# Kernel tuning notes

Measured on AMD Instinct MI355X. Metric: run time of the kernel, lower is better.

The kernel has to match this reference:

```python
import jax, jax.numpy as jnp
import numpy as np

VOCAB = 100000
DIM = 128
BATCH = 16384
NEG = 20
REG = 1e-06


def setup_inputs() -> dict:
    key = jax.random.key(0)
    k1, k2, k3, k4, k5, k6 = jax.random.split(key, 6)
    initrange = 0.5 / DIM
    u_emb = jax.random.uniform(k1, (VOCAB, DIM), jnp.float32, -initrange, initrange)
    # torch init is zeros for v; use small noise so the math is non-degenerate
    v_emb = 0.01 * jax.random.normal(k2, (VOCAB, DIM), jnp.float32)
    # pretrained embeddings given to init_emd (constant numpy array in torch)
    pretrained = jax.random.uniform(k3, (VOCAB, DIM), jnp.float32, -initrange, initrange)
    u_pos = jax.random.randint(k4, (BATCH,), 0, VOCAB)
    v_pos = jax.random.randint(k5, (BATCH,), 0, VOCAB)
    v_neg = jax.random.randint(k6, (BATCH, NEG), 0, VOCAB)
    return {"u_emb": u_emb, "v_emb": v_emb, "pretrained": pretrained,
            "u_pos": u_pos, "v_pos": v_pos, "v_neg": v_neg, "batch_size": BATCH}


def reference(u_emb, v_emb, pretrained, u_pos, v_pos, v_neg, batch_size):
    embed_u = u_emb[u_pos]                      # [B, D]
    embed_v = v_emb[v_pos]                      # [B, D]
    score = jnp.sum(embed_u * embed_v, axis=1)  # [B]
    log_target = jax.nn.log_sigmoid(score)      # [B]

    neg_embed_v = v_emb[v_neg]                              # [B, N, D]
    neg_score = jnp.einsum('bnd,bd->bn', neg_embed_v, embed_u)  # [B, N]
    sum_log_sampled = jnp.sum(jax.nn.log_sigmoid(-neg_score), axis=1)  # [B]

    loss = log_target + sum_log_sampled          # [B]

    # Original python loop: for each j in u_pos, loss += reg * sum|U[j]-P[j]|
    # (scalar broadcast-added to the whole [B] vector each iteration).
    reg_total = REG * jnp.sum(jnp.abs(embed_u - pretrained[u_pos]))  # scalar
    loss = loss + reg_total                      # broadcast, same as the loop

    return -jnp.sum(loss) / batch_size
```

## Files before the change

### kernel.cpp

```cpp
#include <hip/hip_runtime.h>
#include <math.h>

#define NEGS 20
#define DIMS 128
#define REGC 1e-6f
#define LPR  16
#define RPW  4

__device__ __forceinline__ float log_sigmoid(float x) {
    float t = __expf(-fabsf(x));
    float l = -__logf(1.f + t);
    return x >= 0.f ? l : x + l;
}

__device__ __forceinline__ float dot4(float4 a, float4 b) {
    return a.x*b.x + a.y*b.y + a.z*b.z + a.w*b.w;
}

__global__ __launch_bounds__(256) void sg_loss_kernel(
    const float* __restrict__ u_emb,
    const float* __restrict__ v_emb,
    const float* __restrict__ pretrained,
    const int* __restrict__ u_pos,
    const int* __restrict__ v_pos,
    const int* __restrict__ v_neg,
    float* __restrict__ out,
    int batch)
{
    const int lane = threadIdx.x & 63;
    const int l    = lane & (LPR - 1);
    const int g    = lane >> 4;
    const int wib  = threadIdx.x >> 6;
    const int wpb  = blockDim.x >> 6;
    const int gwave  = blockIdx.x * wpb + wib;
    const int nwaves = gridDim.x * wpb;

    float s1 = 0.f;
    float s2 = 0.f;

    for (int base = gwave * RPW; base < batch; base += nwaves * RPW) {
        const int  b     = base + g;
        const bool valid = (b < batch);
        const int  ib    = valid ? b : 0;

        const int iu = u_pos[ib];
        const int iv = v_pos[ib];

        int negidx[NEGS];
        #pragma unroll
        for (int n = 0; n < NEGS; ++n) negidx[n] = v_neg[ib * NEGS + n];

        const float4* up = (const float4*)(u_emb      + (size_t)iu * DIMS);
        const float4* vp = (const float4*)(v_emb      + (size_t)iv * DIMS);
        const float4* pp = (const float4*)(pretrained + (size_t)iu * DIMS);
        const float4 u0 = up[l], u1 = up[l + 16];
        const float4 v0 = vp[l], v1 = vp[l + 16];
        const float4 p0 = pp[l], p1 = pp[l + 16];

        float part[NEGS + 1];
        part[0] = dot4(u0, v0) + dot4(u1, v1);
        #pragma unroll
        for (int n = 0; n < NEGS; ++n) {
            const float4* np = (const float4*)(v_emb + (size_t)negidx[n] * DIMS);
            const float4 a = np[l], c = np[l + 16];
            part[n + 1] = dot4(u0, a) + dot4(u1, c);
        }
        float rp = fabsf(u0.x - p0.x) + fabsf(u0.y - p0.y)
                 + fabsf(u0.z - p0.z) + fabsf(u0.w - p0.w)
                 + fabsf(u1.x - p1.x) + fabsf(u1.y - p1.y)
                 + fabsf(u1.z - p1.z) + fabsf(u1.w - p1.w);

        #pragma unroll
        for (int off = 8; off > 0; off >>= 1) {
            #pragma unroll
            for (int k = 0; k <= NEGS; ++k) part[k] += __shfl_xor(part[k], off, 16);
            rp += __shfl_xor(rp, off, 16);
        }

        float acc = log_sigmoid(part[0]);
        #pragma unroll
        for (int n = 0; n < NEGS; ++n) acc += log_sigmoid(-part[n + 1]);

        if (!valid) { acc = 0.f; rp = 0.f; }
        s1 += acc;
        s2 += rp;
    }

    s1 += __shfl_xor(s1, 16, 64);  s2 += __shfl_xor(s2, 16, 64);
    s1 += __shfl_xor(s1, 32, 64);  s2 += __shfl_xor(s2, 32, 64);

    __shared__ float ls1[8], ls2[8];
    if (lane == 0) { ls1[wib] = s1; ls2[wib] = s2; }
    __syncthreads();
    if (threadIdx.x == 0) {
        float t1 = 0.f, t2 = 0.f;
        for (int w = 0; w < wpb; ++w) { t1 += ls1[w]; t2 += ls2[w]; }
        const float contrib = -(t1 / (float)batch) - REGC * t2;
        atomicAdd(out, contrib);
    }
}

extern "C" void kernel_launch(void* const* d_in, const int* in_sizes, int n_in,
                              void* d_out, int out_size, void* d_ws, size_t ws_size,
                              hipStream_t stream) {
    const float* u_emb      = (const float*)d_in[0];
    const float* v_emb      = (const float*)d_in[1];
    const float* pretrained = (const float*)d_in[2];
    const int*   u_pos      = (const int*)d_in[3];
    const int*   v_pos      = (const int*)d_in[4];
    const int*   v_neg      = (const int*)d_in[5];
    float* out = (float*)d_out;
    const int batch = in_sizes[3];

    hipMemsetAsync(out, 0, sizeof(float), stream);

    dim3 block(256);
    int nwaves = (batch + RPW - 1) / RPW;
    int blocks = (nwaves + 3) / 4;
    sg_loss_kernel<<<dim3(blocks), block, 0, stream>>>(u_emb, v_emb, pretrained,
                                                       u_pos, v_pos, v_neg, out, batch);
}
```

Measured before the change: 46.81 us.

## Split each row's negatives across two waves and drop the grid-stride loop

Each batch row's 20 negative samples are now divided between two waves, ten each. The first wave also handles the positive score and the regularization term. This doubles the number of waves and halves the per-thread register arrays, and launch bounds now request higher occupancy, so more gathers are in flight to hide memory latency. The cost is that the u row is loaded twice, the two waves do unequal work, and twice as many blocks perform atomics.

```diff
diff --git a/kernel.cpp b/kernel.cpp
--- a/kernel.cpp
+++ b/kernel.cpp
@@ -6,6 +6,7 @@
 #define REGC 1e-6f
 #define LPR  16
 #define RPW  4
+#define HNEG 10
 
 __device__ __forceinline__ float log_sigmoid(float x) {
     float t = __expf(-fabsf(x));
@@ -17,7 +18,7 @@
     return a.x*b.x + a.y*b.y + a.z*b.z + a.w*b.w;
 }
 
-__global__ __launch_bounds__(256) void sg_loss_kernel(
+__global__ __launch_bounds__(256, 8) void sg_loss_kernel(
     const float* __restrict__ u_emb,
     const float* __restrict__ v_emb,
     const float* __restrict__ pretrained,
@@ -32,64 +33,68 @@
     const int g    = lane >> 4;
     const int wib  = threadIdx.x >> 6;
     const int wpb  = blockDim.x >> 6;
-    const int gwave  = blockIdx.x * wpb + wib;
-    const int nwaves = gridDim.x * wpb;
+    const int gwave = blockIdx.x * wpb + wib;
 
-    float s1 = 0.f;
-    float s2 = 0.f;
+    const int pair = gwave >> 1;
+    const int half = gwave & 1;
 
-    for (int base = gwave * RPW; base < batch; base += nwaves * RPW) {
-        const int  b     = base + g;
-        const bool valid = (b < batch);
-        const int  ib    = valid ? b : 0;
+    const int  b     = pair * RPW + g;
+    const bool valid = (b < batch);
+    const int  ib    = valid ? b : 0;
 
-        const int iu = u_pos[ib];
+    const int iu = u_pos[ib];
+    const float4* up = (const float4*)(u_emb + (size_t)iu * DIMS);
+    const float4 u0 = up[l], u1 = up[l + 16];
+
+    int negidx[HNEG];
+    const int nb = ib * NEGS + half * HNEG;
+    #pragma unroll
+    for (int n = 0; n < HNEG; ++n) negidx[n] = v_neg[nb + n];
+
+    float part[HNEG + 1];
+    float rp = 0.f;
+    if (half == 0) {
         const int iv = v_pos[ib];
-
-        int negidx[NEGS];
-        #pragma unroll
-        for (int n = 0; n < NEGS; ++n) negidx[n] = v_neg[ib * NEGS + n];
-
-        const float4* up = (const float4*)(u_emb      + (size_t)iu * DIMS);
         const float4* vp = (const float4*)(v_emb      + (size_t)iv * DIMS);
         const float4* pp = (const float4*)(pretrained + (size_t)iu * DIMS);
-        const float4 u0 = up[l], u1 = up[l + 16];
         const float4 v0 = vp[l], v1 = vp[l + 16];
+        part[HNEG] = dot4(u0, v0) + dot4(u1, v1);
         const float4 p0 = pp[l], p1 = pp[l + 16];
+        rp = fabsf(u0.x - p0.x) + fabsf(u0.y - p0.y)
+           + fabsf(u0.z - p0.z) + fabsf(u0.w - p0.w)
+           + fabsf(u1.x - p1.x) + fabsf(u1.y - p1.y)
+           + fabsf(u1.z - p1.z) + fabsf(u1.w - p1.w);
+    } else {
+        part[HNEG] = 0.f;
+    }
 
-        float part[NEGS + 1];
-        part[0] = dot4(u0, v0) + dot4(u1, v1);
+    #pragma unroll
+    for (int n = 0; n < HNEG; ++n) {
+        const float4* np = (const float4*)(v_emb + (size_t)negidx[n] * DIMS);
+        const float4 a = np[l], c = np[l + 16];
+        part[n] = dot4(u0, a) + dot4(u1, c);
+    }
+
+    #pragma unroll
+    for (int off = 8; off > 0; off >>= 1) {
         #pragma unroll
-        for (int n = 0; n < NEGS; ++n) {
-            const float4* np = (const float4*)(v_emb + (size_t)negidx[n] * DIMS);
-            const float4 a = np[l], c = np[l + 16];
-            part[n + 1] = dot4(u0, a) + dot4(u1, c);
-        }
-        float rp = fabsf(u0.x - p0.x) + fabsf(u0.y - p0.y)
-                 + fabsf(u0.z - p0.z) + fabsf(u0.w - p0.w)
-                 + fabsf(u1.x - p1.x) + fabsf(u1.y - p1.y)
-                 + fabsf(u1.z - p1.z) + fabsf(u1.w - p1.w);
+        for (int k = 0; k <= HNEG; ++k) part[k] += __shfl_xor(part[k], off, 16);
+        rp += __shfl_xor(rp, off, 16);
+    }
 
-        #pragma unroll
-        for (int off = 8; off > 0; off >>= 1) {
-            #pragma unroll
-            for (int k = 0; k <= NEGS; ++k) part[k] += __shfl_xor(part[k], off, 16);
-            rp += __shfl_xor(rp, off, 16);
-        }
+    float acc = 0.f;
+    #pragma unroll
+    for (int n = 0; n < HNEG; ++n) acc += log_sigmoid(-part[n]);
+    if (half == 0) acc += log_sigmoid(part[HNEG]);
 
-        float acc = log_sigmoid(part[0]);
-        #pragma unroll
-        for (int n = 0; n < NEGS; ++n) acc += log_sigmoid(-part[n + 1]);
-
-        if (!valid) { acc = 0.f; rp = 0.f; }
-        s1 += acc;
-        s2 += rp;
-    }
+    if (!valid) { acc = 0.f; rp = 0.f; }
+    float s1 = acc;
+    float s2 = rp;
 
     s1 += __shfl_xor(s1, 16, 64);  s2 += __shfl_xor(s2, 16, 64);
     s1 += __shfl_xor(s1, 32, 64);  s2 += __shfl_xor(s2, 32, 64);
 
-    __shared__ float ls1[8], ls2[8];
+    __shared__ float ls1[4], ls2[4];
     if (lane == 0) { ls1[wib] = s1; ls2[wib] = s2; }
     __syncthreads();
     if (threadIdx.x == 0) {
@@ -115,7 +120,7 @@
     hipMemsetAsync(out, 0, sizeof(float), stream);
 
     dim3 block(256);
-    int nwaves = (batch + RPW - 1) / RPW;
+    int nwaves = 2 * ((batch + RPW - 1) / RPW);
     int blocks = (nwaves + 3) / 4;
     sg_loss_kernel<<<dim3(blocks), block, 0, stream>>>(u_emb, v_emb, pretrained,
                                                        u_pos, v_pos, v_neg, out, batch);
```

Measured after the change: 51.40 us. 1.1x slower.

## Use one-wave blocks and batch all negative-row loads before computing

Applied to the files above, without the earlier changes.

Each block is now a single 64-lane wave that handles 4 rows, so the grid-stride loop and the shared-memory block reduction go away. All 40 float4 loads for the negative rows are issued into register arrays before any dot product, which exposes more memory-level parallelism per wave. The cost is much higher register pressure, and therefore possibly lower occupancy, plus one atomicAdd per wave (4096 in total) instead of one per 256-thread block.

```diff
diff --git a/kernel.cpp b/kernel.cpp
--- a/kernel.cpp
+++ b/kernel.cpp
@@ -17,7 +17,7 @@
     return a.x*b.x + a.y*b.y + a.z*b.z + a.w*b.w;
 }
 
-__global__ __launch_bounds__(256) void sg_loss_kernel(
+__global__ void sg_loss_kernel(
     const float* __restrict__ u_emb,
     const float* __restrict__ v_emb,
     const float* __restrict__ pretrained,
@@ -27,75 +27,66 @@
     float* __restrict__ out,
     int batch)
 {
-    const int lane = threadIdx.x & 63;
+    const int lane = threadIdx.x;
     const int l    = lane & (LPR - 1);
     const int g    = lane >> 4;
-    const int wib  = threadIdx.x >> 6;
-    const int wpb  = blockDim.x >> 6;
-    const int gwave  = blockIdx.x * wpb + wib;
-    const int nwaves = gridDim.x * wpb;
 
-    float s1 = 0.f;
-    float s2 = 0.f;
+    const int  b     = blockIdx.x * RPW + g;
+    const bool valid = (b < batch);
+    const int  ib    = valid ? b : 0;
 
-    for (int base = gwave * RPW; base < batch; base += nwaves * RPW) {
-        const int  b     = base + g;
-        const bool valid = (b < batch);
-        const int  ib    = valid ? b : 0;
+    const int iu = u_pos[ib];
+    const int iv = v_pos[ib];
 
-        const int iu = u_pos[ib];
-        const int iv = v_pos[ib];
+    int negidx[NEGS];
+    #pragma unroll
+    for (int n = 0; n < NEGS; ++n) negidx[n] = v_neg[ib * NEGS + n];
 
-        int negidx[NEGS];
+    const float4* up = (const float4*)(u_emb      + (size_t)iu * DIMS);
+    const float4* vp = (const float4*)(v_emb      + (size_t)iv * DIMS);
+    const float4* pp = (const float4*)(pretrained + (size_t)iu * DIMS);
+
+    const float4 u0 = up[l], u1 = up[l + 16];
+    const float4 v0 = vp[l], v1 = vp[l + 16];
+    const float4 p0 = pp[l], p1 = pp[l + 16];
+    float4 a[NEGS], c[NEGS];
+    #pragma unroll
+    for (int n = 0; n < NEGS; ++n) {
+        const float4* np = (const float4*)(v_emb + (size_t)negidx[n] * DIMS);
+        a[n] = np[l];
+        c[n] = np[l + 16];
+    }
+
+    float part[NEGS + 1];
+    part[0] = dot4(u0, v0) + dot4(u1, v1);
+    #pragma unroll
+    for (int n = 0; n < NEGS; ++n) part[n + 1] = dot4(u0, a[n]) + dot4(u1, c[n]);
+
+    float rp = fabsf(u0.x - p0.x) + fabsf(u0.y - p0.y)
+             + fabsf(u0.z - p0.z) + fabsf(u0.w - p0.w)
+             + fabsf(u1.x - p1.x) + fabsf(u1.y - p1.y)
+             + fabsf(u1.z - p1.z) + fabsf(u1.w - p1.w);
+
+    #pragma unroll
+    for (int off = 8; off > 0; off >>= 1) {
         #pragma unroll
-        for (int n = 0; n < NEGS; ++n) negidx[n] = v_neg[ib * NEGS + n];
+        for (int k = 0; k <= NEGS; ++k) part[k] += __shfl_xor(part[k], off, 16);
+        rp += __shfl_xor(rp, off, 16);
+    }
 
-        const float4* up = (const float4*)(u_emb      + (size_t)iu * DIMS);
-        const float4* vp = (const float4*)(v_emb      + (size_t)iv * DIMS);
-        const float4* pp = (const float4*)(pretrained + (size_t)iu * DIMS);
-        const float4 u0 = up[l], u1 = up[l + 16];
-        const float4 v0 = vp[l], v1 = vp[l + 16];
-        const float4 p0 = pp[l], p1 = pp[l + 16];
+    float acc = log_sigmoid(part[0]);
+    #pragma unroll
+    for (int n = 0; n < NEGS; ++n) acc += log_sigmoid(-part[n + 1]);
 
-        float part[NEGS + 1];
-        part[0] = dot4(u0, v0) + dot4(u1, v1);
-        #pragma unroll
-        for (int n = 0; n < NEGS; ++n) {
-            const float4* np = (const float4*)(v_emb + (size_t)negidx[n] * DIMS);
-            const float4 a = np[l], c = np[l + 16];
-            part[n + 1] = dot4(u0, a) + dot4(u1, c);
-        }
-        float rp = fabsf(u0.x - p0.x) + fabsf(u0.y - p0.y)
-                 + fabsf(u0.z - p0.z) + fabsf(u0.w - p0.w)
-                 + fabsf(u1.x - p1.x) + fabsf(u1.y - p1.y)
-                 + fabsf(u1.z - p1.z) + fabsf(u1.w - p1.w);
-
-        #pragma unroll
-        for (int off = 8; off > 0; off >>= 1) {
-            #pragma unroll
-            for (int k = 0; k <= NEGS; ++k) part[k] += __shfl_xor(part[k], off, 16);
-            rp += __shfl_xor(rp, off, 16);
-        }
-
-        float acc = log_sigmoid(part[0]);
-        #pragma unroll
-        for (int n = 0; n < NEGS; ++n) acc += log_sigmoid(-part[n + 1]);
-
-        if (!valid) { acc = 0.f; rp = 0.f; }
-        s1 += acc;
-        s2 += rp;
-    }
+    if (!valid) { acc = 0.f; rp = 0.f; }
+    float s1 = acc;
+    float s2 = rp;
 
     s1 += __shfl_xor(s1, 16, 64);  s2 += __shfl_xor(s2, 16, 64);
     s1 += __shfl_xor(s1, 32, 64);  s2 += __shfl_xor(s2, 32, 64);
 
-    __shared__ float ls1[8], ls2[8];
-    if (lane == 0) { ls1[wib] = s1; ls2[wib] = s2; }
-    __syncthreads();
-    if (threadIdx.x == 0) {
-        float t1 = 0.f, t2 = 0.f;
-        for (int w = 0; w < wpb; ++w) { t1 += ls1[w]; t2 += ls2[w]; }
-        const float contrib = -(t1 / (float)batch) - REGC * t2;
+    if (lane == 0) {
+        const float contrib = -(s1 / (float)batch) - REGC * s2;
         atomicAdd(out, contrib);
     }
 }
@@ -114,9 +105,8 @@
 
     hipMemsetAsync(out, 0, sizeof(float), stream);
 
-    dim3 block(256);
-    int nwaves = (batch + RPW - 1) / RPW;
-    int blocks = (nwaves + 3) / 4;
+    dim3 block(64);
+    int blocks = (batch + RPW - 1) / RPW;
     sg_loss_kernel<<<dim3(blocks), block, 0, stream>>>(u_emb, v_emb, pretrained,
                                                        u_pos, v_pos, v_neg, out, batch);
 }
```

New measurement: 77.68 us. 66.0% more time.
